# Kernel optimization log

Hardware: AMD Instinct MI355X
Metric: run time of the kernel (lower is better)

## Reference

```python
import jax, jax.numpy as jnp
import numpy as np

N = 50000
E = 400000
F_IN = 128
NUM_CLASSES = 16
# (heads, out_channels, concat) per GATConv layer
LAYERS = [(8, 32, True), (8, 16, True), (8, 8, True), (1, NUM_CLASSES, False)]
DIMS_IN = [F_IN, 256, 128, 64]
NEG_SLOPE = 0.2
BN_EPS = 1e-5


def setup_inputs() -> dict:
    key = jax.random.key(0)
    ks = iter(jax.random.split(key, 64))
    inp = {}
    inp["x"] = jax.random.normal(next(ks), (N, F_IN), dtype=jnp.float32)
    inp["src"] = jax.random.randint(next(ks), (E,), 0, N, dtype=jnp.int32)
    inp["dst"] = jax.random.randint(next(ks), (E,), 0, N, dtype=jnp.int32)
    for l, ((h, c, concat), din) in enumerate(zip(LAYERS, DIMS_IN), start=1):
        s = 1.0 / np.sqrt(din)
        inp[f"W{l}"] = jax.random.normal(next(ks), (din, h * c), dtype=jnp.float32) * s
        inp[f"asrc{l}"] = jax.random.normal(next(ks), (h, c), dtype=jnp.float32) * 0.1
        inp[f"adst{l}"] = jax.random.normal(next(ks), (h, c), dtype=jnp.float32) * 0.1
        dout = h * c if concat else c
        inp[f"b{l}"] = jax.random.normal(next(ks), (dout,), dtype=jnp.float32) * 0.01
        inp[f"g{l}"] = jax.random.uniform(next(ks), (dout,), dtype=jnp.float32, minval=0.5, maxval=1.5)
        inp[f"be{l}"] = jax.random.normal(next(ks), (dout,), dtype=jnp.float32) * 0.1
        inp[f"rm{l}"] = jax.random.normal(next(ks), (dout,), dtype=jnp.float32) * 0.1
        inp[f"rv{l}"] = jax.random.uniform(next(ks), (dout,), dtype=jnp.float32, minval=0.5, maxval=1.5)
    return inp


def _gat_conv(x, src, dst, W, a_src, a_dst, bias, heads, ch, concat):
    n = x.shape[0]
    h = (x @ W).reshape(n, heads, ch)                     # [N,H,C]
    e_s = jnp.einsum('nhc,hc->nh', h, a_src)              # [N,H]
    e_d = jnp.einsum('nhc,hc->nh', h, a_dst)
    alpha = jax.nn.leaky_relu(e_s[src] + e_d[dst], NEG_SLOPE)   # [E,H]
    amax = jax.ops.segment_max(alpha, dst, num_segments=n)
    ex = jnp.exp(alpha - amax[dst])
    den = jax.ops.segment_sum(ex, dst, num_segments=n)
    attn = ex / (den[dst] + 1e-16)                        # [E,H]
    out = jax.ops.segment_sum(h[src] * attn[:, :, None], dst, num_segments=n)  # [N,H,C]
    out = out.reshape(n, heads * ch) if concat else out.mean(axis=1)
    return out + bias


def _bn(x, g, b, rm, rv):
    return (x - rm) * jax.lax.rsqrt(rv + BN_EPS) * g + b


def _forward(x, src, dst, params):
    # PyG GATConv adds self-loops by default
    loops = jnp.arange(N, dtype=src.dtype)
    s = jnp.concatenate([src, loops])
    d = jnp.concatenate([dst, loops])
    out = x
    for l, (h, c, concat) in enumerate(LAYERS, start=1):
        W, a_s, a_d, b, g, be, rm, rv = (params[f"{k}{l}"] for k in
                                         ("W", "asrc", "adst", "b", "g", "be", "rm", "rv"))
        out = _gat_conv(out, s, d, W, a_s, a_d, b, h, c, concat)
        if l < 4:
            out = jax.nn.elu(out)
        out = _bn(out, g, be, rm, rv)
    return out


def reference(x, src, dst,
              W1, asrc1, adst1, b1, g1, be1, rm1, rv1,
              W2, asrc2, adst2, b2, g2, be2, rm2, rv2,
              W3, asrc3, adst3, b3, g3, be3, rm3, rv3,
              W4, asrc4, adst4, b4, g4, be4, rm4, rv4):
    params = dict(
        W1=W1, asrc1=asrc1, adst1=adst1, b1=b1, g1=g1, be1=be1, rm1=rm1, rv1=rv1,
        W2=W2, asrc2=asrc2, adst2=adst2, b2=b2, g2=g2, be2=be2, rm2=rm2, rv2=rv2,
        W3=W3, asrc3=asrc3, adst3=adst3, b3=b3, g3=g3, be3=be3, rm3=rm3, rv3=rv3,
        W4=W4, asrc4=asrc4, adst4=adst4, b4=b4, g4=g4, be4=be4, rm4=rm4, rv4=rv4)
    return _forward(x, src, dst, params)
```

## Files before the change

### kernel.cpp

```cpp
#include <hip/hip_runtime.h>

#define NEG_SLOPE 0.2f
#define BN_EPS 1e-5f

typedef unsigned short u16;
typedef unsigned int u32;
typedef __bf16 bf16x8 __attribute__((ext_vector_type(8)));
typedef float f32x4 __attribute__((ext_vector_type(4)));

__device__ __forceinline__ u32 f2bf(float f) {
    u32 u = __float_as_uint(f);
    return (u + 0x7FFFu + ((u >> 16) & 1u)) >> 16;
}
__device__ __forceinline__ float bf2f(u32 h) { return __uint_as_float(h << 16); }
__device__ __forceinline__ float bfl(u32 p) { return __uint_as_float(p << 16); }
__device__ __forceinline__ float bfh(u32 p) { return __uint_as_float(p & 0xFFFF0000u); }

__global__ void split_kernel(const float4* __restrict__ X, uint2* __restrict__ hi,
                             uint2* __restrict__ lo, int n4) {
    int i = blockIdx.x * blockDim.x + threadIdx.x;
    if (i >= n4) return;
    float4 v = X[i];
    u32 h0 = f2bf(v.x), h1 = f2bf(v.y), h2 = f2bf(v.z), h3 = f2bf(v.w);
    hi[i] = make_uint2(h0 | (h1 << 16), h2 | (h3 << 16));
    u32 l0 = f2bf(v.x - bf2f(h0)), l1 = f2bf(v.y - bf2f(h1)),
        l2 = f2bf(v.z - bf2f(h2)), l3 = f2bf(v.w - bf2f(h3));
    lo[i] = make_uint2(l0 | (l1 << 16), l2 | (l3 << 16));
}

__global__ void wt_prep(const float* __restrict__ W, u16* __restrict__ hi,
                        u16* __restrict__ lo, int K, int N) {
    int i = blockIdx.x * blockDim.x + threadIdx.x;
    if (i >= K * N) return;
    int k = i / N, n = i - k * N;
    float w = W[i];
    u32 h = f2bf(w);
    hi[n * K + k] = (u16)h;
    lo[n * K + k] = (u16)f2bf(w - bf2f(h));
}

template<int BN, int HMC>
__launch_bounds__(256)
__global__ void gemm_mfma(const u16* __restrict__ Ahi, const u16* __restrict__ Alo,
                          const u16* __restrict__ Bhi, const u16* __restrict__ Blo,
                          u16* __restrict__ Cbf, int M, int K, int N) {
    constexpr int FM = (BN == 128) ? 4 : 2;
    __shared__ uint4 sA[2][512];
    __shared__ uint4 sB[2][BN * 4];
    const int tid = threadIdx.x;
    const int bm = blockIdx.y * 128;
    const int bn = blockIdx.x * BN;
    const int lane = tid & 63;
    const int w = tid >> 6;
    const int wm = (BN == 128) ? (w >> 1) * 64 : w * 32;
    const int wn = (BN == 128) ? (w & 1) * 64 : 0;
    const int fr = lane & 15;
    const int fs = lane >> 4;
    f32x4 zero = {0.f, 0.f, 0.f, 0.f};
    f32x4 acc[FM][4];
    #pragma unroll
    for (int i = 0; i < FM; i++)
        #pragma unroll
        for (int j = 0; j < 4; j++) acc[i][j] = zero;

    const int r0 = tid >> 2;
    const int ss = tid & 3;
    const int r1 = r0 + 64;
    const int d0 = r0 * 4 + (ss ^ ((r0 >> 1) & 3));
    const int d1 = r1 * 4 + (ss ^ ((r1 >> 1) & 3));

    for (int k0 = 0; k0 < K; k0 += 32) {
        {
            int gr = bm + r0;
            uint4 vh = make_uint4(0, 0, 0, 0), vl = make_uint4(0, 0, 0, 0);
            if (gr < M) {
                vh = *(const uint4*)(Ahi + (size_t)gr * K + k0 + ss * 8);
                vl = *(const uint4*)(Alo + (size_t)gr * K + k0 + ss * 8);
            }
            sA[0][d0] = vh; sA[1][d0] = vl;
            gr = bm + r1;
            vh = make_uint4(0, 0, 0, 0); vl = make_uint4(0, 0, 0, 0);
            if (gr < M) {
                vh = *(const uint4*)(Ahi + (size_t)gr * K + k0 + ss * 8);
                vl = *(const uint4*)(Alo + (size_t)gr * K + k0 + ss * 8);
            }
            sA[0][d1] = vh; sA[1][d1] = vl;
        }
        {
            int gr = bn + r0;
            sB[0][d0] = *(const uint4*)(Bhi + (size_t)gr * K + k0 + ss * 8);
            sB[1][d0] = *(const uint4*)(Blo + (size_t)gr * K + k0 + ss * 8);
            if constexpr (BN == 128) {
                gr = bn + r1;
                sB[0][d1] = *(const uint4*)(Bhi + (size_t)gr * K + k0 + ss * 8);
                sB[1][d1] = *(const uint4*)(Blo + (size_t)gr * K + k0 + ss * 8);
            }
        }
        __syncthreads();
        bf16x8 ah[FM], al[FM], bh[4], bl[4];
        #pragma unroll
        for (int mi = 0; mi < FM; mi++) {
            int row = wm + mi * 16 + fr;
            int idx = row * 4 + (fs ^ ((row >> 1) & 3));
            ah[mi] = *reinterpret_cast<const bf16x8*>(&sA[0][idx]);
            al[mi] = *reinterpret_cast<const bf16x8*>(&sA[1][idx]);
        }
        #pragma unroll
        for (int ni = 0; ni < 4; ni++) {
            int row = wn + ni * 16 + fr;
            int idx = row * 4 + (fs ^ ((row >> 1) & 3));
            bh[ni] = *reinterpret_cast<const bf16x8*>(&sB[0][idx]);
            bl[ni] = *reinterpret_cast<const bf16x8*>(&sB[1][idx]);
        }
        #pragma unroll
        for (int mi = 0; mi < FM; mi++)
            #pragma unroll
            for (int ni = 0; ni < 4; ni++) {
                acc[mi][ni] = __builtin_amdgcn_mfma_f32_16x16x32_bf16(ah[mi], bh[ni], acc[mi][ni], 0, 0, 0);
                acc[mi][ni] = __builtin_amdgcn_mfma_f32_16x16x32_bf16(ah[mi], bl[ni], acc[mi][ni], 0, 0, 0);
                acc[mi][ni] = __builtin_amdgcn_mfma_f32_16x16x32_bf16(al[mi], bh[ni], acc[mi][ni], 0, 0, 0);
            }
        __syncthreads();
    }
    #pragma unroll
    for (int mi = 0; mi < FM; mi++) {
        #pragma unroll
        for (int ni = 0; ni < 4; ni++) {
            int colg = bn + wn + ni * 16 + fr;
            int rbase = bm + wm + mi * 16 + fs * 4;
            #pragma unroll
            for (int r = 0; r < 4; r++) {
                int rw = rbase + r;
                if (rw >= M) continue;
                u16 val = (u16)f2bf(acc[mi][ni][r]);
                if constexpr (HMC > 0) {
                    int hh2 = colg / HMC, cc2 = colg - hh2 * HMC;
                    Cbf[((size_t)hh2 * M + rw) * HMC + cc2] = val;
                } else {
                    Cbf[(size_t)rw * N + colg] = val;
                }
            }
        }
    }
}

__launch_bounds__(256)
__global__ void gemm_k64n16(const float* __restrict__ A, const float* __restrict__ B,
                            u16* __restrict__ Cbf, int M) {
    __shared__ float As[64][68];
    __shared__ float Bs[64][16];
    const int tid = threadIdx.x;
    const int bm = blockIdx.x * 64;
    {
        int r = tid >> 2, c = (tid & 3) << 2;
        *reinterpret_cast<float4*>(&Bs[r][c]) = *reinterpret_cast<const float4*>(&B[r * 16 + c]);
    }
    #pragma unroll
    for (int p = 0; p < 4; p++) {
        int m = (tid >> 4) + p * 16;
        int c = (tid & 15) << 2;
        int gm = bm + m;
        float4 v = make_float4(0.f, 0.f, 0.f, 0.f);
        if (gm < M) v = *reinterpret_cast<const float4*>(&A[(size_t)gm * 64 + c]);
        *reinterpret_cast<float4*>(&As[m][c]) = v;
    }
    __syncthreads();
    const int tc = tid & 15;
    const int r0 = tid >> 4;
    float acc[4] = {};
    #pragma unroll
    for (int k4 = 0; k4 < 16; k4++) {
        float b0 = Bs[4 * k4 + 0][tc];
        float b1 = Bs[4 * k4 + 1][tc];
        float b2 = Bs[4 * k4 + 2][tc];
        float b3 = Bs[4 * k4 + 3][tc];
        #pragma unroll
        for (int i = 0; i < 4; i++) {
            float4 av = *reinterpret_cast<const float4*>(&As[r0 + i * 16][4 * k4]);
            acc[i] += av.x * b0 + av.y * b1 + av.z * b2 + av.w * b3;
        }
    }
    #pragma unroll
    for (int i = 0; i < 4; i++) {
        int m = bm + r0 + i * 16;
        if (m < M) Cbf[(size_t)m * 16 + tc] = (u16)f2bf(acc[i]);
    }
}

__global__ void scores_kernel(const u16* __restrict__ h,
                              const float* __restrict__ asrc,
                              const float* __restrict__ adst,
                              float* __restrict__ es, float* __restrict__ ed,
                              int Nn, int H, int C) {
    int idx = blockIdx.x * blockDim.x + threadIdx.x;
    if (idx >= Nn * H) return;
    int n = idx / H, hh = idx % H;
    const u16* hp = h + ((size_t)hh * Nn + n) * C;
    const float4* ap = reinterpret_cast<const float4*>(asrc + hh * C);
    const float4* bp = reinterpret_cast<const float4*>(adst + hh * C);
    float s = 0.f, d = 0.f;
    for (int c4 = 0; c4 < C / 4; c4++) {
        uint2 pv = *reinterpret_cast<const uint2*>(hp + 4 * c4);
        float v0 = bfl(pv.x), v1 = bfh(pv.x), v2 = bfl(pv.y), v3 = bfh(pv.y);
        float4 a = ap[c4], b = bp[c4];
        s += v0 * a.x + v1 * a.y + v2 * a.z + v3 * a.w;
        d += v0 * b.x + v1 * b.y + v2 * b.z + v3 * b.w;
    }
    es[(size_t)hh * Nn + n] = s;
    ed[(size_t)hh * Nn + n] = d;
}

__global__ void hist_kernel(const int* __restrict__ dst, int* __restrict__ counts,
                            int E0, int Etot) {
    int e = blockIdx.x * blockDim.x + threadIdx.x;
    if (e >= Etot) return;
    int d_ = (e < E0) ? dst[e] : e - E0;
    atomicAdd(&counts[d_], 1);
}

__global__ void scan_kernel(const int* __restrict__ counts, int* __restrict__ row_ptr, int Nn) {
    __shared__ int wsum[16];
    __shared__ int chunk_total;
    __shared__ int carry_s;
    const int tid = threadIdx.x;
    const int lane = tid & 63;
    const int wid = tid >> 6;
    if (tid == 0) carry_s = 0;
    __syncthreads();
    for (int base = 0; base < Nn; base += 1024) {
        int i = base + tid;
        int v = (i < Nn) ? counts[i] : 0;
        int iv = v;
        #pragma unroll
        for (int off = 1; off < 64; off <<= 1) {
            int t = __shfl_up(iv, off, 64);
            if (lane >= off) iv += t;
        }
        if (lane == 63) wsum[wid] = iv;
        __syncthreads();
        if (tid == 0) {
            int s = 0;
            #pragma unroll
            for (int k = 0; k < 16; k++) { int t = wsum[k]; wsum[k] = s; s += t; }
            chunk_total = s;
        }
        __syncthreads();
        if (i < Nn) row_ptr[i] = carry_s + wsum[wid] + (iv - v);
        __syncthreads();
        if (tid == 0) carry_s += chunk_total;
        __syncthreads();
    }
    if (tid == 0) row_ptr[Nn] = carry_s;
}

__global__ void scatter_kernel(const int* __restrict__ src, const int* __restrict__ dst,
                               int* __restrict__ cursor, int* __restrict__ col,
                               int E0, int Etot) {
    int e = blockIdx.x * blockDim.x + threadIdx.x;
    if (e >= Etot) return;
    int d_ = (e < E0) ? dst[e] : e - E0;
    int s_ = (e < E0) ? src[e] : e - E0;
    int pos = atomicAdd(&cursor[d_], 1);
    col[pos] = s_;
}

template<int H, int C, int NT, int DO_ELU, int OUT_HILO>
__launch_bounds__(256)
__global__ void gat_fused(const int* __restrict__ row_ptr, const int* __restrict__ col,
                          const float* __restrict__ es, const float* __restrict__ ed,
                          const u16* __restrict__ h16, float* __restrict__ outf,
                          u16* __restrict__ outh, u16* __restrict__ outl,
                          const float* __restrict__ bias, const float* __restrict__ g,
                          const float* __restrict__ be, const float* __restrict__ rm,
                          const float* __restrict__ rv, int Nn) {
    constexpr int Dout = H * C;
    constexpr int NPB = 256 / NT;
    const int tid = threadIdx.x;
    const int node = blockIdx.x * NPB + tid / NT;
    const int t = tid % NT;
    const int hh = blockIdx.y;
    if (node >= Nn) return;
    const int jb = row_ptr[node], je = row_ptr[node + 1];
    const float* esh = es + (size_t)hh * Nn;
    const float edv = ed[(size_t)hh * Nn + node];
    const u16* hb = h16 + (size_t)hh * Nn * C + t * 4;
    float a0c = 0.f, a1c = 0.f, a2c = 0.f, a3c = 0.f, den = 0.f;
    int j = jb;
    for (; j + 4 <= je; j += 4) {
        int s0 = col[j], s1 = col[j + 1], s2 = col[j + 2], s3 = col[j + 3];
        float e0 = esh[s0] + edv, e1 = esh[s1] + edv, e2 = esh[s2] + edv, e3 = esh[s3] + edv;
        uint2 p0 = *reinterpret_cast<const uint2*>(hb + (size_t)s0 * C);
        uint2 p1 = *reinterpret_cast<const uint2*>(hb + (size_t)s1 * C);
        uint2 p2 = *reinterpret_cast<const uint2*>(hb + (size_t)s2 * C);
        uint2 p3 = *reinterpret_cast<const uint2*>(hb + (size_t)s3 * C);
        e0 = (e0 >= 0.f) ? e0 : NEG_SLOPE * e0;
        e1 = (e1 >= 0.f) ? e1 : NEG_SLOPE * e1;
        e2 = (e2 >= 0.f) ? e2 : NEG_SLOPE * e2;
        e3 = (e3 >= 0.f) ? e3 : NEG_SLOPE * e3;
        float w0 = __expf(e0), w1 = __expf(e1), w2 = __expf(e2), w3 = __expf(e3);
        den += (w0 + w1) + (w2 + w3);
        a0c += w0 * bfl(p0.x) + w1 * bfl(p1.x) + w2 * bfl(p2.x) + w3 * bfl(p3.x);
        a1c += w0 * bfh(p0.x) + w1 * bfh(p1.x) + w2 * bfh(p2.x) + w3 * bfh(p3.x);
        a2c += w0 * bfl(p0.y) + w1 * bfl(p1.y) + w2 * bfl(p2.y) + w3 * bfl(p3.y);
        a3c += w0 * bfh(p0.y) + w1 * bfh(p1.y) + w2 * bfh(p2.y) + w3 * bfh(p3.y);
    }
    for (; j < je; j++) {
        int s = col[j];
        float a = esh[s] + edv;
        a = (a >= 0.f) ? a : NEG_SLOPE * a;
        float w = __expf(a);
        uint2 pv = *reinterpret_cast<const uint2*>(hb + (size_t)s * C);
        den += w;
        a0c += w * bfl(pv.x); a1c += w * bfh(pv.x);
        a2c += w * bfl(pv.y); a3c += w * bfh(pv.y);
    }
    const float inv = 1.f / (den + 1e-16f);
    const int jc = hh * C + t * 4;
    float res[4] = {a0c, a1c, a2c, a3c};
    #pragma unroll
    for (int v = 0; v < 4; v++) {
        float y = res[v] * inv + bias[jc + v];
        if (DO_ELU) y = (y > 0.f) ? y : expm1f(y);
        y = (y - rm[jc + v]) * rsqrtf(rv[jc + v] + BN_EPS) * g[jc + v] + be[jc + v];
        res[v] = y;
    }
    if constexpr (OUT_HILO) {
        u32 rh[4], rl[4];
        #pragma unroll
        for (int v = 0; v < 4; v++) {
            rh[v] = f2bf(res[v]);
            rl[v] = f2bf(res[v] - bf2f(rh[v]));
        }
        uint2 ph = make_uint2(rh[0] | (rh[1] << 16), rh[2] | (rh[3] << 16));
        uint2 pl = make_uint2(rl[0] | (rl[1] << 16), rl[2] | (rl[3] << 16));
        *reinterpret_cast<uint2*>(outh + (size_t)node * Dout + jc) = ph;
        *reinterpret_cast<uint2*>(outl + (size_t)node * Dout + jc) = pl;
    } else {
        *reinterpret_cast<float4*>(outf + (size_t)node * Dout + jc) =
            make_float4(res[0], res[1], res[2], res[3]);
    }
}

extern "C" void kernel_launch(void* const* d_in, const int* in_sizes, int n_in,
                              void* d_out, int out_size, void* d_ws, size_t ws_size,
                              hipStream_t stream) {
    const float* x = (const float*)d_in[0];
    const int* src = (const int*)d_in[1];
    const int* dst = (const int*)d_in[2];
    const int Nn = in_sizes[0] / 128;
    const int E0 = in_sizes[1];
    const int Etot = E0 + Nn;

    u16* A0 = (u16*)d_ws;
    u16* Bh = A0 + (size_t)Nn * 512;
    u16* Ch = Bh + (size_t)Nn * 256;
    float* es = (float*)(Ch + (size_t)Nn * 256);
    float* ed = es + (size_t)Nn * 8;
    int* row_ptr = (int*)(ed + (size_t)Nn * 8);
    int* cursor  = row_ptr + (Nn + 1);
    int* col     = cursor + Nn;
    u16* wth = (u16*)(col + Etot);
    u16* wtl = wth + 65536;

    u16* XH = A0;
    u16* XL = A0 + (size_t)Nn * 128;
    u16* Y1H = A0;
    u16* Y1L = A0 + (size_t)Nn * 256;
    u16* Y2H = Ch;
    u16* Y2L = Ch + (size_t)Nn * 128;
    float* out3 = (float*)A0;

    hipMemsetAsync(cursor, 0, sizeof(int) * Nn, stream);
    hist_kernel<<<(Etot + 255) / 256, 256, 0, stream>>>(dst, cursor, E0, Etot);
    scan_kernel<<<1, 1024, 0, stream>>>(cursor, row_ptr, Nn);
    hipMemcpyAsync(cursor, row_ptr, sizeof(int) * Nn, hipMemcpyDeviceToDevice, stream);
    scatter_kernel<<<(Etot + 255) / 256, 256, 0, stream>>>(src, dst, cursor, col, E0, Etot);

    const int gy128 = (Nn + 127) / 128;

    for (int l = 0; l < 4; l++) {
        const float* const* p = (const float* const*)(d_in + 3 + l * 8);
        const float* W    = p[0];
        const float* asrc = p[1];
        const float* adst = p[2];
        const float* bias = p[3];
        const float* g    = p[4];
        const float* be   = p[5];
        const float* rm   = p[6];
        const float* rv   = p[7];

        if (l == 0) {
            const int K = 128, N = 256;
            int n4 = Nn * K / 4;
            split_kernel<<<(n4 + 255) / 256, 256, 0, stream>>>(
                (const float4*)x, (uint2*)XH, (uint2*)XL, n4);
            wt_prep<<<(K * N + 255) / 256, 256, 0, stream>>>(W, wth, wtl, K, N);
            gemm_mfma<128, 32><<<dim3(N / 128, gy128), 256, 0, stream>>>(XH, XL, wth, wtl, Bh, Nn, K, N);
            scores_kernel<<<(Nn * 8 + 255) / 256, 256, 0, stream>>>(Bh, asrc, adst, es, ed, Nn, 8, 32);
            gat_fused<8, 32, 8, 1, 1><<<dim3((Nn + 31) / 32, 8), 256, 0, stream>>>(
                row_ptr, col, es, ed, Bh, nullptr, Y1H, Y1L, bias, g, be, rm, rv, Nn);
        } else if (l == 1) {
            const int K = 256, N = 128;
            wt_prep<<<(K * N + 255) / 256, 256, 0, stream>>>(W, wth, wtl, K, N);
            gemm_mfma<128, 16><<<dim3(1, gy128), 256, 0, stream>>>(Y1H, Y1L, wth, wtl, Bh, Nn, K, N);
            scores_kernel<<<(Nn * 8 + 255) / 256, 256, 0, stream>>>(Bh, asrc, adst, es, ed, Nn, 8, 16);
            gat_fused<8, 16, 4, 1, 1><<<dim3((Nn + 63) / 64, 8), 256, 0, stream>>>(
                row_ptr, col, es, ed, Bh, nullptr, Y2H, Y2L, bias, g, be, rm, rv, Nn);
        } else if (l == 2) {
            const int K = 128, N = 64;
            wt_prep<<<(K * N + 255) / 256, 256, 0, stream>>>(W, wth, wtl, K, N);
            gemm_mfma<64, 8><<<dim3(1, gy128), 256, 0, stream>>>(Y2H, Y2L, wth, wtl, Bh, Nn, K, N);
            scores_kernel<<<(Nn * 8 + 255) / 256, 256, 0, stream>>>(Bh, asrc, adst, es, ed, Nn, 8, 8);
            gat_fused<8, 8, 2, 1, 0><<<dim3((Nn + 127) / 128, 8), 256, 0, stream>>>(
                row_ptr, col, es, ed, Bh, out3, nullptr, nullptr, bias, g, be, rm, rv, Nn);
        } else {
            gemm_k64n16<<<(Nn + 63) / 64, 256, 0, stream>>>(out3, W, Bh, Nn);
            scores_kernel<<<(Nn + 255) / 256, 256, 0, stream>>>(Bh, asrc, adst, es, ed, Nn, 1, 16);
            gat_fused<1, 16, 4, 0, 0><<<dim3((Nn + 63) / 64, 1), 256, 0, stream>>>(
                row_ptr, col, es, ed, Bh, (float*)d_out, nullptr, nullptr, bias, g, be, rm, rv, Nn);
        }
    }
}
```

Measured before the change: 405.3 us.

## Precompute fp16 edge attention weights, fuse input split into GEMM, batch weight prep

Result: slower. 491.6 us (+21.3%).

```diff
diff --git a/kernel.cpp b/kernel.cpp
--- a/kernel.cpp
+++ b/kernel.cpp
@@ -15,33 +15,39 @@
 __device__ __forceinline__ float bf2f(u32 h) { return __uint_as_float(h << 16); }
 __device__ __forceinline__ float bfl(u32 p) { return __uint_as_float(p << 16); }
 __device__ __forceinline__ float bfh(u32 p) { return __uint_as_float(p & 0xFFFF0000u); }
-
-__global__ void split_kernel(const float4* __restrict__ X, uint2* __restrict__ hi,
-                             uint2* __restrict__ lo, int n4) {
+__device__ __forceinline__ u16 f2h(float f) { _Float16 h = (_Float16)f; return *(u16*)&h; }
+__device__ __forceinline__ float h2f(u16 u) { _Float16 h = *(_Float16*)&u; return (float)h; }
+
+__device__ __forceinline__ void split8(const float4 f0, const float4 f1, uint4& vh, uint4& vl) {
+    float f[8] = {f0.x, f0.y, f0.z, f0.w, f1.x, f1.y, f1.z, f1.w};
+    u32 h[8], l[8];
+    #pragma unroll
+    for (int i = 0; i < 8; i++) { h[i] = f2bf(f[i]); l[i] = f2bf(f[i] - bf2f(h[i])); }
+    vh = make_uint4(h[0] | (h[1] << 16), h[2] | (h[3] << 16), h[4] | (h[5] << 16), h[6] | (h[7] << 16));
+    vl = make_uint4(l[0] | (l[1] << 16), l[2] | (l[3] << 16), l[4] | (l[5] << 16), l[6] | (l[7] << 16));
+}
+
+__global__ void wt_prep3(const float* __restrict__ W1, const float* __restrict__ W2,
+                         const float* __restrict__ W3,
+                         u16* __restrict__ h1, u16* __restrict__ l1,
+                         u16* __restrict__ h2, u16* __restrict__ l2,
+                         u16* __restrict__ h3, u16* __restrict__ l3) {
     int i = blockIdx.x * blockDim.x + threadIdx.x;
-    if (i >= n4) return;
-    float4 v = X[i];
-    u32 h0 = f2bf(v.x), h1 = f2bf(v.y), h2 = f2bf(v.z), h3 = f2bf(v.w);
-    hi[i] = make_uint2(h0 | (h1 << 16), h2 | (h3 << 16));
-    u32 l0 = f2bf(v.x - bf2f(h0)), l1 = f2bf(v.y - bf2f(h1)),
-        l2 = f2bf(v.z - bf2f(h2)), l3 = f2bf(v.w - bf2f(h3));
-    lo[i] = make_uint2(l0 | (l1 << 16), l2 | (l3 << 16));
-}
-
-__global__ void wt_prep(const float* __restrict__ W, u16* __restrict__ hi,
-                        u16* __restrict__ lo, int K, int N) {
-    int i = blockIdx.x * blockDim.x + threadIdx.x;
-    if (i >= K * N) return;
-    int k = i / N, n = i - k * N;
-    float w = W[i];
+    const float* W; u16 *ph, *pl; int K, N, off;
+    if (i < 32768)      { W = W1; ph = h1; pl = l1; K = 128; N = 256; off = i; }
+    else if (i < 65536) { W = W2; ph = h2; pl = l2; K = 256; N = 128; off = i - 32768; }
+    else if (i < 73728) { W = W3; ph = h3; pl = l3; K = 128; N = 64;  off = i - 65536; }
+    else return;
+    int k = off / N, n = off - k * N;
+    float w = W[off];
     u32 h = f2bf(w);
-    hi[n * K + k] = (u16)h;
-    lo[n * K + k] = (u16)f2bf(w - bf2f(h));
-}
-
-template<int BN, int HMC>
+    ph[n * K + k] = (u16)h;
+    pl[n * K + k] = (u16)f2bf(w - bf2f(h));
+}
+
+template<int BN, int HMC, int AF32>
 __launch_bounds__(256)
-__global__ void gemm_mfma(const u16* __restrict__ Ahi, const u16* __restrict__ Alo,
+__global__ void gemm_mfma(const void* __restrict__ A_, const u16* __restrict__ Alo,
                           const u16* __restrict__ Bhi, const u16* __restrict__ Blo,
                           u16* __restrict__ Cbf, int M, int K, int N) {
     constexpr int FM = (BN == 128) ? 4 : 2;
@@ -70,16 +76,35 @@
     const int d1 = r1 * 4 + (ss ^ ((r1 >> 1) & 3));
 
     for (int k0 = 0; k0 < K; k0 += 32) {
-        {
+        if constexpr (AF32) {
+            const float* Af = (const float*)A_;
             int gr = bm + r0;
-            uint4 vh = make_uint4(0, 0, 0, 0), vl = make_uint4(0, 0, 0, 0);
+            uint4 vh = make_uint4(0,0,0,0), vl = make_uint4(0,0,0,0);
+            if (gr < M) {
+                float4 f0 = *(const float4*)(Af + (size_t)gr * K + k0 + ss * 8);
+                float4 f1 = *(const float4*)(Af + (size_t)gr * K + k0 + ss * 8 + 4);
+                split8(f0, f1, vh, vl);
+            }
+            sA[0][d0] = vh; sA[1][d0] = vl;
+            gr = bm + r1;
+            vh = make_uint4(0,0,0,0); vl = make_uint4(0,0,0,0);
+            if (gr < M) {
+                float4 f0 = *(const float4*)(Af + (size_t)gr * K + k0 + ss * 8);
+                float4 f1 = *(const float4*)(Af + (size_t)gr * K + k0 + ss * 8 + 4);
+                split8(f0, f1, vh, vl);
+            }
+            sA[0][d1] = vh; sA[1][d1] = vl;
+        } else {
+            const u16* Ahi = (const u16*)A_;
+            int gr = bm + r0;
+            uint4 vh = make_uint4(0,0,0,0), vl = make_uint4(0,0,0,0);
             if (gr < M) {
                 vh = *(const uint4*)(Ahi + (size_t)gr * K + k0 + ss * 8);
                 vl = *(const uint4*)(Alo + (size_t)gr * K + k0 + ss * 8);
             }
             sA[0][d0] = vh; sA[1][d0] = vl;
             gr = bm + r1;
-            vh = make_uint4(0, 0, 0, 0); vl = make_uint4(0, 0, 0, 0);
+            vh = make_uint4(0,0,0,0); vl = make_uint4(0,0,0,0);
             if (gr < M) {
                 vh = *(const uint4*)(Ahi + (size_t)gr * K + k0 + ss * 8);
                 vl = *(const uint4*)(Alo + (size_t)gr * K + k0 + ss * 8);
@@ -206,8 +231,8 @@
         s += v0 * a.x + v1 * a.y + v2 * a.z + v3 * a.w;
         d += v0 * b.x + v1 * b.y + v2 * b.z + v3 * b.w;
     }
-    es[(size_t)hh * Nn + n] = s;
-    ed[(size_t)hh * Nn + n] = d;
+    es[(size_t)n * H + hh] = s;
+    ed[(size_t)n * H + hh] = d;
 }
 
 __global__ void hist_kernel(const int* __restrict__ dst, int* __restrict__ counts,
@@ -218,7 +243,7 @@
     atomicAdd(&counts[d_], 1);
 }
 
-__global__ void scan_kernel(const int* __restrict__ counts, int* __restrict__ row_ptr, int Nn) {
+__global__ void scan_kernel(int* __restrict__ counts, int* __restrict__ row_ptr, int Nn) {
     __shared__ int wsum[16];
     __shared__ int chunk_total;
     __shared__ int carry_s;
@@ -245,7 +270,11 @@
             chunk_total = s;
         }
         __syncthreads();
-        if (i < Nn) row_ptr[i] = carry_s + wsum[wid] + (iv - v);
+        if (i < Nn) {
+            int ex = carry_s + wsum[wid] + (iv - v);
+            row_ptr[i] = ex;
+            counts[i] = ex;
+        }
         __syncthreads();
         if (tid == 0) carry_s += chunk_total;
         __syncthreads();
@@ -264,12 +293,75 @@
     col[pos] = s_;
 }
 
+__global__ void edge_w8(const int* __restrict__ row_ptr, const int* __restrict__ col,
+                        const float* __restrict__ es, const float* __restrict__ ed,
+                        u16* __restrict__ attn, int Nn) {
+    int n = blockIdx.x * blockDim.x + threadIdx.x;
+    if (n >= Nn) return;
+    const int jb = row_ptr[n], je = row_ptr[n + 1];
+    float4 e0 = *reinterpret_cast<const float4*>(ed + (size_t)n * 8);
+    float4 e1 = *reinterpret_cast<const float4*>(ed + (size_t)n * 8 + 4);
+    float edv[8] = {e0.x, e0.y, e0.z, e0.w, e1.x, e1.y, e1.z, e1.w};
+    float den[8] = {};
+    for (int j = jb; j < je; j++) {
+        int s = col[j];
+        float4 q0 = *reinterpret_cast<const float4*>(es + (size_t)s * 8);
+        float4 q1 = *reinterpret_cast<const float4*>(es + (size_t)s * 8 + 4);
+        float q[8] = {q0.x, q0.y, q0.z, q0.w, q1.x, q1.y, q1.z, q1.w};
+        #pragma unroll
+        for (int h = 0; h < 8; h++) {
+            float a = q[h] + edv[h];
+            a = (a >= 0.f) ? a : NEG_SLOPE * a;
+            den[h] += __expf(a);
+        }
+    }
+    float inv[8];
+    #pragma unroll
+    for (int h = 0; h < 8; h++) inv[h] = 1.f / (den[h] + 1e-16f);
+    for (int j = jb; j < je; j++) {
+        int s = col[j];
+        float4 q0 = *reinterpret_cast<const float4*>(es + (size_t)s * 8);
+        float4 q1 = *reinterpret_cast<const float4*>(es + (size_t)s * 8 + 4);
+        float q[8] = {q0.x, q0.y, q0.z, q0.w, q1.x, q1.y, q1.z, q1.w};
+        u16 wv[8];
+        #pragma unroll
+        for (int h = 0; h < 8; h++) {
+            float a = q[h] + edv[h];
+            a = (a >= 0.f) ? a : NEG_SLOPE * a;
+            wv[h] = f2h(__expf(a) * inv[h]);
+        }
+        uint4 pk = make_uint4((u32)wv[0] | ((u32)wv[1] << 16), (u32)wv[2] | ((u32)wv[3] << 16),
+                              (u32)wv[4] | ((u32)wv[5] << 16), (u32)wv[6] | ((u32)wv[7] << 16));
+        *reinterpret_cast<uint4*>(attn + (size_t)j * 8) = pk;
+    }
+}
+
+__global__ void edge_w1(const int* __restrict__ row_ptr, const int* __restrict__ col,
+                        const float* __restrict__ es, const float* __restrict__ ed,
+                        u16* __restrict__ attn, int Nn) {
+    int n = blockIdx.x * blockDim.x + threadIdx.x;
+    if (n >= Nn) return;
+    const int jb = row_ptr[n], je = row_ptr[n + 1];
+    const float edv = ed[n];
+    float den = 0.f;
+    for (int j = jb; j < je; j++) {
+        float a = es[col[j]] + edv;
+        a = (a >= 0.f) ? a : NEG_SLOPE * a;
+        den += __expf(a);
+    }
+    float inv = 1.f / (den + 1e-16f);
+    for (int j = jb; j < je; j++) {
+        float a = es[col[j]] + edv;
+        a = (a >= 0.f) ? a : NEG_SLOPE * a;
+        attn[j] = f2h(__expf(a) * inv);
+    }
+}
+
 template<int H, int C, int NT, int DO_ELU, int OUT_HILO>
 __launch_bounds__(256)
 __global__ void gat_fused(const int* __restrict__ row_ptr, const int* __restrict__ col,
-                          const float* __restrict__ es, const float* __restrict__ ed,
-                          const u16* __restrict__ h16, float* __restrict__ outf,
-                          u16* __restrict__ outh, u16* __restrict__ outl,
+                          const u16* __restrict__ attn, const u16* __restrict__ h16,
+                          float* __restrict__ outf, u16* __restrict__ outh, u16* __restrict__ outl,
                           const float* __restrict__ bias, const float* __restrict__ g,
                           const float* __restrict__ be, const float* __restrict__ rm,
                           const float* __restrict__ rv, int Nn) {
@@ -281,45 +373,35 @@
     const int hh = blockIdx.y;
     if (node >= Nn) return;
     const int jb = row_ptr[node], je = row_ptr[node + 1];
-    const float* esh = es + (size_t)hh * Nn;
-    const float edv = ed[(size_t)hh * Nn + node];
     const u16* hb = h16 + (size_t)hh * Nn * C + t * 4;
-    float a0c = 0.f, a1c = 0.f, a2c = 0.f, a3c = 0.f, den = 0.f;
+    float a0 = 0.f, a1 = 0.f, a2 = 0.f, a3 = 0.f;
     int j = jb;
-    for (; j + 4 <= je; j += 4) {
-        int s0 = col[j], s1 = col[j + 1], s2 = col[j + 2], s3 = col[j + 3];
-        float e0 = esh[s0] + edv, e1 = esh[s1] + edv, e2 = esh[s2] + edv, e3 = esh[s3] + edv;
-        uint2 p0 = *reinterpret_cast<const uint2*>(hb + (size_t)s0 * C);
-        uint2 p1 = *reinterpret_cast<const uint2*>(hb + (size_t)s1 * C);
-        uint2 p2 = *reinterpret_cast<const uint2*>(hb + (size_t)s2 * C);
-        uint2 p3 = *reinterpret_cast<const uint2*>(hb + (size_t)s3 * C);
-        e0 = (e0 >= 0.f) ? e0 : NEG_SLOPE * e0;
-        e1 = (e1 >= 0.f) ? e1 : NEG_SLOPE * e1;
-        e2 = (e2 >= 0.f) ? e2 : NEG_SLOPE * e2;
-        e3 = (e3 >= 0.f) ? e3 : NEG_SLOPE * e3;
-        float w0 = __expf(e0), w1 = __expf(e1), w2 = __expf(e2), w3 = __expf(e3);
-        den += (w0 + w1) + (w2 + w3);
-        a0c += w0 * bfl(p0.x) + w1 * bfl(p1.x) + w2 * bfl(p2.x) + w3 * bfl(p3.x);
-        a1c += w0 * bfh(p0.x) + w1 * bfh(p1.x) + w2 * bfh(p2.x) + w3 * bfh(p3.x);
-        a2c += w0 * bfl(p0.y) + w1 * bfl(p1.y) + w2 * bfl(p2.y) + w3 * bfl(p3.y);
-        a3c += w0 * bfh(p0.y) + w1 * bfh(p1.y) + w2 * bfh(p2.y) + w3 * bfh(p3.y);
+    for (; j + 8 <= je; j += 8) {
+        int s[8]; float w[8]; uint2 p[8];
+        #pragma unroll
+        for (int u = 0; u < 8; u++) s[u] = col[j + u];
+        #pragma unroll
+        for (int u = 0; u < 8; u++) w[u] = h2f(attn[(size_t)(j + u) * H + hh]);
+        #pragma unroll
+        for (int u = 0; u < 8; u++) p[u] = *reinterpret_cast<const uint2*>(hb + (size_t)s[u] * C);
+        #pragma unroll
+        for (int u = 0; u < 8; u++) {
+            a0 += w[u] * bfl(p[u].x); a1 += w[u] * bfh(p[u].x);
+            a2 += w[u] * bfl(p[u].y); a3 += w[u] * bfh(p[u].y);
+        }
     }
     for (; j < je; j++) {
         int s = col[j];
-        float a = esh[s] + edv;
-        a = (a >= 0.f) ? a : NEG_SLOPE * a;
-        float w = __expf(a);
+        float w = h2f(attn[(size_t)j * H + hh]);
         uint2 pv = *reinterpret_cast<const uint2*>(hb + (size_t)s * C);
-        den += w;
-        a0c += w * bfl(pv.x); a1c += w * bfh(pv.x);
-        a2c += w * bfl(pv.y); a3c += w * bfh(pv.y);
-    }
-    const float inv = 1.f / (den + 1e-16f);
+        a0 += w * bfl(pv.x); a1 += w * bfh(pv.x);
+        a2 += w * bfl(pv.y); a3 += w * bfh(pv.y);
+    }
     const int jc = hh * C + t * 4;
-    float res[4] = {a0c, a1c, a2c, a3c};
+    float res[4] = {a0, a1, a2, a3};
     #pragma unroll
     for (int v = 0; v < 4; v++) {
-        float y = res[v] * inv + bias[jc + v];
+        float y = res[v] + bias[jc + v];
         if (DO_ELU) y = (y > 0.f) ? y : expm1f(y);
         y = (y - rm[jc + v]) * rsqrtf(rv[jc + v] + BN_EPS) * g[jc + v] + be[jc + v];
         res[v] = y;
@@ -359,11 +441,14 @@
     int* row_ptr = (int*)(ed + (size_t)Nn * 8);
     int* cursor  = row_ptr + (Nn + 1);
     int* col     = cursor + Nn;
-    u16* wth = (u16*)(col + Etot);
-    u16* wtl = wth + 65536;
-
-    u16* XH = A0;
-    u16* XL = A0 + (size_t)Nn * 128;
+    u16* wth1 = (u16*)(col + Etot);
+    u16* wtl1 = wth1 + 32768;
+    u16* wth2 = wtl1 + 32768;
+    u16* wtl2 = wth2 + 32768;
+    u16* wth3 = wtl2 + 32768;
+    u16* wtl3 = wth3 + 8192;
+    u16* attn = wtl3 + 8192;
+
     u16* Y1H = A0;
     u16* Y1L = A0 + (size_t)Nn * 256;
     u16* Y2H = Ch;
@@ -373,51 +458,38 @@
     hipMemsetAsync(cursor, 0, sizeof(int) * Nn, stream);
     hist_kernel<<<(Etot + 255) / 256, 256, 0, stream>>>(dst, cursor, E0, Etot);
     scan_kernel<<<1, 1024, 0, stream>>>(cursor, row_ptr, Nn);
-    hipMemcpyAsync(cursor, row_ptr, sizeof(int) * Nn, hipMemcpyDeviceToDevice, stream);
     scatter_kernel<<<(Etot + 255) / 256, 256, 0, stream>>>(src, dst, cursor, col, E0, Etot);
 
     const int gy128 = (Nn + 127) / 128;
 
-    for (int l = 0; l < 4; l++) {
-        const float* const* p = (const float* const*)(d_in + 3 + l * 8);
-        const float* W    = p[0];
-        const float* asrc = p[1];
-        const float* adst = p[2];
-        const float* bias = p[3];
-        const float* g    = p[4];
-        const float* be   = p[5];
-        const float* rm   = p[6];
-        const float* rv   = p[7];
-
-        if (l == 0) {
-            const int K = 128, N = 256;
-            int n4 = Nn * K / 4;
-            split_kernel<<<(n4 + 255) / 256, 256, 0, stream>>>(
-                (const float4*)x, (uint2*)XH, (uint2*)XL, n4);
-            wt_prep<<<(K * N + 255) / 256, 256, 0, stream>>>(W, wth, wtl, K, N);
-            gemm_mfma<128, 32><<<dim3(N / 128, gy128), 256, 0, stream>>>(XH, XL, wth, wtl, Bh, Nn, K, N);
-            scores_kernel<<<(Nn * 8 + 255) / 256, 256, 0, stream>>>(Bh, asrc, adst, es, ed, Nn, 8, 32);
-            gat_fused<8, 32, 8, 1, 1><<<dim3((Nn + 31) / 32, 8), 256, 0, stream>>>(
-                row_ptr, col, es, ed, Bh, nullptr, Y1H, Y1L, bias, g, be, rm, rv, Nn);
-        } else if (l == 1) {
-            const int K = 256, N = 128;
-            wt_prep<<<(K * N + 255) / 256, 256, 0, stream>>>(W, wth, wtl, K, N);
-            gemm_mfma<128, 16><<<dim3(1, gy128), 256, 0, stream>>>(Y1H, Y1L, wth, wtl, Bh, Nn, K, N);
-            scores_kernel<<<(Nn * 8 + 255) / 256, 256, 0, stream>>>(Bh, asrc, adst, es, ed, Nn, 8, 16);
-            gat_fused<8, 16, 4, 1, 1><<<dim3((Nn + 63) / 64, 8), 256, 0, stream>>>(
-                row_ptr, col, es, ed, Bh, nullptr, Y2H, Y2L, bias, g, be, rm, rv, Nn);
-        } else if (l == 2) {
-            const int K = 128, N = 64;
-            wt_prep<<<(K * N + 255) / 256, 256, 0, stream>>>(W, wth, wtl, K, N);
-            gemm_mfma<64, 8><<<dim3(1, gy128), 256, 0, stream>>>(Y2H, Y2L, wth, wtl, Bh, Nn, K, N);
-            scores_kernel<<<(Nn * 8 + 255) / 256, 256, 0, stream>>>(Bh, asrc, adst, es, ed, Nn, 8, 8);
-            gat_fused<8, 8, 2, 1, 0><<<dim3((Nn + 127) / 128, 8), 256, 0, stream>>>(
-                row_ptr, col, es, ed, Bh, out3, nullptr, nullptr, bias, g, be, rm, rv, Nn);
-        } else {
-            gemm_k64n16<<<(Nn + 63) / 64, 256, 0, stream>>>(out3, W, Bh, Nn);
-            scores_kernel<<<(Nn + 255) / 256, 256, 0, stream>>>(Bh, asrc, adst, es, ed, Nn, 1, 16);
-            gat_fused<1, 16, 4, 0, 0><<<dim3((Nn + 63) / 64, 1), 256, 0, stream>>>(
-                row_ptr, col, es, ed, Bh, (float*)d_out, nullptr, nullptr, bias, g, be, rm, rv, Nn);
-        }
-    }
-}
+    const float* const* p1 = (const float* const*)(d_in + 3);
+    const float* const* p2 = (const float* const*)(d_in + 11);
+    const float* const* p3 = (const float* const*)(d_in + 19);
+    const float* const* p4 = (const float* const*)(d_in + 27);
+
+    wt_prep3<<<288, 256, 0, stream>>>(p1[0], p2[0], p3[0], wth1, wtl1, wth2, wtl2, wth3, wtl3);
+
+    gemm_mfma<128, 32, 1><<<dim3(2, gy128), 256, 0, stream>>>(x, nullptr, wth1, wtl1, Bh, Nn, 128, 256);
+    scores_kernel<<<(Nn * 8 + 255) / 256, 256, 0, stream>>>(Bh, p1[1], p1[2], es, ed, Nn, 8, 32);
+    edge_w8<<<(Nn + 255) / 256, 256, 0, stream>>>(row_ptr, col, es, ed, attn, Nn);
+    gat_fused<8, 32, 8, 1, 1><<<dim3((Nn + 31) / 32, 8), 256, 0, stream>>>(
+        row_ptr, col, attn, Bh, nullptr, Y1H, Y1L, p1[3], p1[4], p1[5], p1[6], p1[7], Nn);
+
+    gemm_mfma<128, 16, 0><<<dim3(1, gy128), 256, 0, stream>>>(Y1H, Y1L, wth2, wtl2, Bh, Nn, 256, 128);
+    scores_kernel<<<(Nn * 8 + 255) / 256, 256, 0, stream>>>(Bh, p2[1], p2[2], es, ed, Nn, 8, 16);
+    edge_w8<<<(Nn + 255) / 256, 256, 0, stream>>>(row_ptr, col, es, ed, attn, Nn);
+    gat_fused<8, 16, 4, 1, 1><<<dim3((Nn + 63) / 64, 8), 256, 0, stream>>>(
+        row_ptr, col, attn, Bh, nullptr, Y2H, Y2L, p2[3], p2[4], p2[5], p2[6], p2[7], Nn);
+
+    gemm_mfma<64, 8, 0><<<dim3(1, gy128), 256, 0, stream>>>(Y2H, Y2L, wth3, wtl3, Bh, Nn, 128, 64);
+    scores_kernel<<<(Nn * 8 + 255) / 256, 256, 0, stream>>>(Bh, p3[1], p3[2], es, ed, Nn, 8, 8);
+    edge_w8<<<(Nn + 255) / 256, 256, 0, stream>>>(row_ptr, col, es, ed, attn, Nn);
+    gat_fused<8, 8, 2, 1, 0><<<dim3((Nn + 127) / 128, 8), 256, 0, stream>>>(
+        row_ptr, col, attn, Bh, out3, nullptr, nullptr, p3[3], p3[4], p3[5], p3[6], p3[7], Nn);
+
+    gemm_k64n16<<<(Nn + 63) / 64, 256, 0, stream>>>(out3, p4[0], Bh, Nn);
+    scores_kernel<<<(Nn + 255) / 256, 256, 0, stream>>>(Bh, p4[1], p4[2], es, ed, Nn, 1, 16);
+    edge_w1<<<(Nn + 255) / 256, 256, 0, stream>>>(row_ptr, col, es, ed, attn, Nn);
+    gat_fused<1, 16, 4, 0, 0><<<dim3((Nn + 63) / 64, 1), 256, 0, stream>>>(
+        row_ptr, col, attn, Bh, (float*)d_out, nullptr, nullptr, p4[3], p4[4], p4[5], p4[6], p4[7], Nn);
+}
```
